# Kernel tuning notes

Hardware: AMD Instinct MI355X
Metric: run time of the kernel (lower is better)

The kernel has to match this reference:

```python
import jax, jax.numpy as jnp
import numpy as np

# AutoNCP(units=512, output_size=64) layer sizes (per ncps AutoNCP formula):
# inter_and_command = 512-64 = 448; command = max(int(0.4*448),1) = 179;
# inter = 448-179 = 269; motor = 64.
INPUT_DIM = 74  # LATENT(64)+ACTION(8)+CLICK(2), hard-coded in source
INTER, COMMAND, MOTOR = 269, 179, 64
BATCH = 65536
DENSITY = 0.5  # AutoNCP default density_level


def _make_layer(key, in_dim, hid):
    # CfCCell params (backbone_layers=0 => cat_shape = in_dim + hid).
    ks = jax.random.split(key, 9)
    s = 1.0 / np.sqrt(in_dim + hid)
    def W(k):
        return jax.random.uniform(k, (in_dim + hid, hid), minval=-s, maxval=s, dtype=jnp.float32)
    def b(k):
        return jax.random.uniform(k, (hid,), minval=-s, maxval=s, dtype=jnp.float32)
    # sparsity mask: sensory/inter part is sparse (~density), recurrent part is all ones
    # (WiredCfCCell concatenates a ones block for the hidden-state columns).
    top = (jax.random.uniform(ks[8], (in_dim, hid)) < DENSITY).astype(jnp.int32)
    mask = jnp.concatenate([top, jnp.ones((hid, hid), jnp.int32)], axis=0)  # [in+hid, hid]
    return dict(Wf1=W(ks[0]), bf1=b(ks[1]), Wf2=W(ks[2]), bf2=b(ks[3]),
                Wta=W(ks[4]), bta=b(ks[5]), Wtb=W(ks[6]), btb=b(ks[7]), mask=mask)


def setup_inputs() -> dict:
    key = jax.random.key(0)
    kx, k0, k1, k2 = jax.random.split(key, 4)
    inp = {"x": jax.random.normal(kx, (BATCH, INPUT_DIM), dtype=jnp.float32)}
    for i, (kk, in_dim, hid) in enumerate([(k0, INPUT_DIM, INTER), (k1, INTER, COMMAND), (k2, COMMAND, MOTOR)]):
        p = _make_layer(kk, in_dim, hid)
        for name, v in p.items():
            inp[f"{name}_{i}"] = v
    return inp


def _cfc_cell(x_in, h, mask, Wf1, bf1, Wf2, bf2, Wta, bta, Wtb, btb, ts=1.0):
    # x = cat([input, hx]); ff1/ff2 use sparsity-masked weights; time_a/time_b dense.
    xx = jnp.concatenate([x_in, h], axis=1)           # [B, in+hid]
    m = mask.astype(xx.dtype)
    ff1 = jnp.tanh(xx @ (Wf1 * m) + bf1)
    ff2 = jnp.tanh(xx @ (Wf2 * m) + bf2)
    t_a = xx @ Wta + bta
    t_b = xx @ Wtb + btb
    t_interp = jax.nn.sigmoid(-t_a * ts + t_b)        # closed-form time gate
    return ff1 * (1.0 - t_interp) + t_interp * ff2


def reference(x,
              Wf1_0, bf1_0, Wf2_0, bf2_0, Wta_0, bta_0, Wtb_0, btb_0, mask_0,
              Wf1_1, bf1_1, Wf2_1, bf2_1, Wta_1, bta_1, Wtb_1, btb_1, mask_1,
              Wf1_2, bf1_2, Wf2_2, bf2_2, Wta_2, bta_2, Wtb_2, btb_2, mask_2):
    B = x.shape[0]
    # seq_len = 1, zero initial hidden state, ts = 1.0 (CfC default elapsed time)
    h0 = jnp.zeros((B, INTER), x.dtype)
    h1 = jnp.zeros((B, COMMAND), x.dtype)
    h2 = jnp.zeros((B, MOTOR), x.dtype)
    o0 = _cfc_cell(x,  h0, mask_0, Wf1_0, bf1_0, Wf2_0, bf2_0, Wta_0, bta_0, Wtb_0, btb_0)
    o1 = _cfc_cell(o0, h1, mask_1, Wf1_1, bf1_1, Wf2_1, bf2_1, Wta_1, bta_1, Wtb_1, btb_1)
    o2 = _cfc_cell(o1, h2, mask_2, Wf1_2, bf1_2, Wf2_2, bf2_2, Wta_2, bta_2, Wtb_2, btb_2)
    return o2  # out[:, -1, :] -> motor neurons, [B, 64]
```

## Files before the change

### kernel.cpp

```cpp
#include <hip/hip_runtime.h>
#include <hip/hip_fp16.h>

typedef _Float16 f16x8 __attribute__((ext_vector_type(8)));
typedef _Float16 f16x4 __attribute__((ext_vector_type(4)));
typedef _Float16 f16x2 __attribute__((ext_vector_type(2)));
typedef float    f32x4 __attribute__((ext_vector_type(4)));

#define BM 64

#define IN0 74
#define H0  269
#define H1  179
#define H2  64
#define KS0 3
#define KS1 9
#define KS2 6
#define NP0 272
#define NP1 192
#define NP2 64
#define PX  104
#define PH0 296
#define PH1 200

#define MFMA16(a, b, c) __builtin_amdgcn_mfma_f32_16x16x32_f16(a, b, c, 0, 0, 0)

__device__ __forceinline__ float rform(float y) {
  return __builtin_amdgcn_rcpf(1.f + __expf(y));
}

template<int KS, int NP, int HID, int IPITCH, int OPITCH, bool LAST, int S, int G>
__device__ __forceinline__ void layer_run(
    const _Float16* in_lds, _Float16* out_lds, float* out_g,
    const _Float16* __restrict__ wt, int lane, int wid)
{
  constexpr int NT = NP / 16;
  const int l15 = lane & 15;
  const int lg  = lane >> 4;
  #pragma unroll 1
  for (int u = wid; u < NT * G; u += 8) {
    const int t     = u / G;
    const int mbase = (u % G) * (S * 16);
    const _Float16* a_base = in_lds + (mbase + l15) * IPITCH + lg * 8;
    const _Float16* wtt = wt + (size_t)(t * KS * 3) * 512 + lane * 8;

    f32x4 acc[3][S] = {};
    f16x8 b0 = *(const f16x8*)(wtt);
    f16x8 b1 = *(const f16x8*)(wtt + 512);
    f16x8 b2 = *(const f16x8*)(wtt + 1024);
    #pragma unroll 1
    for (int ks = 0; ks < KS - 1; ++ks) {
      const _Float16* wn = wtt + (size_t)(ks + 1) * 1536;
      f16x8 n0 = *(const f16x8*)(wn);
      f16x8 n1 = *(const f16x8*)(wn + 512);
      f16x8 n2 = *(const f16x8*)(wn + 1024);
      #pragma unroll
      for (int s = 0; s < S; ++s) {
        f16x8 a = *(const f16x8*)(a_base + s * 16 * IPITCH + ks * 32);
        acc[0][s] = MFMA16(b0, a, acc[0][s]);
        acc[1][s] = MFMA16(b1, a, acc[1][s]);
        acc[2][s] = MFMA16(b2, a, acc[2][s]);
      }
      b0 = n0; b1 = n1; b2 = n2;
    }
    #pragma unroll
    for (int s = 0; s < S; ++s) {
      f16x8 a = *(const f16x8*)(a_base + s * 16 * IPITCH + (KS - 1) * 32);
      acc[0][s] = MFMA16(b0, a, acc[0][s]);
      acc[1][s] = MFMA16(b1, a, acc[1][s]);
      acc[2][s] = MFMA16(b2, a, acc[2][s]);
    }

    const int nb = t * 16 + lg * 4;
    #pragma unroll
    for (int s = 0; s < S; ++s) {
      const int m = mbase + s * 16 + l15;
      float o[4];
      #pragma unroll
      for (int q = 0; q < 4; ++q) {
        float r1 = rform(acc[0][s][q]);
        float r2 = rform(acc[1][s][q]);
        float ti = rform(-acc[2][s][q]);
        o[q] = 1.f - 2.f * (r1 - ti * (r1 - r2));
      }
      if (LAST) {
        float4 v = make_float4(o[0], o[1], o[2], o[3]);
        *(float4*)(out_g + m * 64 + nb) = v;
      } else if (nb + 4 <= HID) {
        f16x4 h = {(_Float16)o[0], (_Float16)o[1], (_Float16)o[2], (_Float16)o[3]};
        *(f16x4*)(out_lds + m * OPITCH + nb) = h;
      } else {
        #pragma unroll
        for (int q = 0; q < 4; ++q)
          if (nb + q < HID) out_lds[m * OPITCH + nb + q] = (_Float16)o[q];
      }
    }
  }
}

__global__ __launch_bounds__(512, 4) void cfc_fused(
    const float* __restrict__ x,
    const _Float16* __restrict__ wt0, const _Float16* __restrict__ wt1,
    const _Float16* __restrict__ wt2,
    float* __restrict__ out)
{
  __shared__ __align__(16) _Float16 xs [BM * PX];
  __shared__ __align__(16) _Float16 h0s[BM * PH0];
  __shared__ __align__(16) _Float16 h1s[BM * PH1];
  const int tid  = threadIdx.x;
  const int lane = tid & 63;
  const int wid  = tid >> 6;
  const int m0 = blockIdx.x * BM;

  for (int i = tid; i < BM * 22; i += 512) { int r = i / 22, c = IN0 + i - r * 22; xs [r * PX  + c] = (_Float16)(c == IN0 ? 1.f : 0.f); }
  for (int i = tid; i < BM * 19; i += 512) { int r = i / 19, c = H0  + i - r * 19; h0s[r * PH0 + c] = (_Float16)(c == H0  ? 1.f : 0.f); }
  for (int i = tid; i < BM * 13; i += 512) { int r = i / 13, c = H1  + i - r * 13; h1s[r * PH1 + c] = (_Float16)(c == H1  ? 1.f : 0.f); }

  for (int i = tid; i < BM * 37; i += 512) {
    int r = i / 37, p = i - r * 37;
    float2 v = ((const float2*)x)[(size_t)(m0 + r) * 37 + p];
    f16x2 hv = {(_Float16)v.x, (_Float16)v.y};
    *(f16x2*)(xs + r * PX + 2 * p) = hv;
  }
  __syncthreads();

  layer_run<KS0, NP0, H0, PX,  PH0, false, 4, 1>(xs,  h0s, nullptr, wt0, lane, wid);
  __syncthreads();
  layer_run<KS1, NP1, H1, PH0, PH1, false, 4, 1>(h0s, h1s, nullptr, wt1, lane, wid);
  __syncthreads();
  layer_run<KS2, NP2, H2, PH1, 1,   true,  2, 2>(h1s, nullptr, out + (size_t)m0 * 64,
                                                 wt2, lane, wid);
}

__global__ void pack_w(const float* __restrict__ wf1, const float* __restrict__ wf2,
                       const float* __restrict__ wta, const float* __restrict__ wtb,
                       const float* __restrict__ bf1, const float* __restrict__ bf2,
                       const float* __restrict__ bta, const float* __restrict__ btb,
                       const int* __restrict__ mask, _Float16* __restrict__ wt,
                       int IN, int HID, int KS, int NT)
{
  int idx = blockIdx.x * 256 + threadIdx.x;
  int total = NT * KS * 3 * 64;
  if (idx >= total) return;
  int lane = idx & 63;
  int c = idx >> 6;
  int m = c % 3;
  int tk = c / 3;
  int ks = tk % KS;
  int t  = tk / KS;
  int n  = t * 16 + (lane & 15);
  int k0 = ks * 32 + (lane >> 4) * 8;
  f16x8 v = {};
  if (n < HID) {
    #pragma unroll
    for (int j = 0; j < 8; ++j) {
      int k = k0 + j;
      float f = 0.f;
      if (k < IN) {
        if (m == 0)      f = 2.f * wf1[k * HID + n] * (float)mask[k * HID + n];
        else if (m == 1) f = 2.f * wf2[k * HID + n] * (float)mask[k * HID + n];
        else             f = wtb[k * HID + n] - wta[k * HID + n];
      } else if (k == IN) {
        if (m == 0)      f = 2.f * bf1[n];
        else if (m == 1) f = 2.f * bf2[n];
        else             f = btb[n] - bta[n];
      }
      v[j] = (_Float16)f;
    }
  }
  *(f16x8*)(wt + (size_t)idx * 8) = v;
}

extern "C" void kernel_launch(void* const* d_in, const int* in_sizes, int n_in,
                              void* d_out, int out_size, void* d_ws, size_t ws_size,
                              hipStream_t stream)
{
  const float* x = (const float*)d_in[0];
  const float* Wf1_0 = (const float*)d_in[1];
  const float* bf1_0 = (const float*)d_in[2];
  const float* Wf2_0 = (const float*)d_in[3];
  const float* bf2_0 = (const float*)d_in[4];
  const float* Wta_0 = (const float*)d_in[5];
  const float* bta_0 = (const float*)d_in[6];
  const float* Wtb_0 = (const float*)d_in[7];
  const float* btb_0 = (const float*)d_in[8];
  const int*   msk_0 = (const int*)  d_in[9];
  const float* Wf1_1 = (const float*)d_in[10];
  const float* bf1_1 = (const float*)d_in[11];
  const float* Wf2_1 = (const float*)d_in[12];
  const float* bf2_1 = (const float*)d_in[13];
  const float* Wta_1 = (const float*)d_in[14];
  const float* bta_1 = (const float*)d_in[15];
  const float* Wtb_1 = (const float*)d_in[16];
  const float* btb_1 = (const float*)d_in[17];
  const int*   msk_1 = (const int*)  d_in[18];
  const float* Wf1_2 = (const float*)d_in[19];
  const float* bf1_2 = (const float*)d_in[20];
  const float* Wf2_2 = (const float*)d_in[21];
  const float* bf2_2 = (const float*)d_in[22];
  const float* Wta_2 = (const float*)d_in[23];
  const float* bta_2 = (const float*)d_in[24];
  const float* Wtb_2 = (const float*)d_in[25];
  const float* btb_2 = (const float*)d_in[26];
  const int*   msk_2 = (const int*)  d_in[27];

  char* ws = (char*)d_ws;
  _Float16* wt0 = (_Float16*)(ws + 0);
  _Float16* wt1 = (_Float16*)(ws + 156672);
  _Float16* wt2 = (_Float16*)(ws + 488448);

  pack_w<<<(17 * KS0 * 3 * 64 + 255) / 256, 256, 0, stream>>>(
      Wf1_0, Wf2_0, Wta_0, Wtb_0, bf1_0, bf2_0, bta_0, btb_0, msk_0, wt0, IN0, H0, KS0, 17);
  pack_w<<<(12 * KS1 * 3 * 64 + 255) / 256, 256, 0, stream>>>(
      Wf1_1, Wf2_1, Wta_1, Wtb_1, bf1_1, bf2_1, bta_1, btb_1, msk_1, wt1, H0, H1, KS1, 12);
  pack_w<<<( 4 * KS2 * 3 * 64 + 255) / 256, 256, 0, stream>>>(
      Wf1_2, Wf2_2, Wta_2, Wtb_2, bf1_2, bf2_2, bta_2, btb_2, msk_2, wt2, H1, H2, KS2, 4);

  cfc_fused<<<65536 / BM, 512, 0, stream>>>(x, wt0, wt1, wt2, (float*)d_out);
}
```

Before: 72.56 us.

## Double batch tile to 128 rows, 12 waves, two N-tiles per wave

Each block now handles 128 rows with 768 threads (12 waves), and every wave computes two adjacent 16-column N-tiles, so each A fragment loaded from LDS feeds six MFMAs instead of three. Layer 0 is padded to 288 columns so the tile count is even, and the weight workspace offsets are shifted to match. The double-buffered weight prefetch is dropped in favour of loading all six B fragments per k-step. The accumulator count doubles, which raises register pressure, and the larger LDS footprint plus 768-thread blocks lowers the number of resident blocks per CU.

```diff
diff --git a/kernel.cpp b/kernel.cpp
--- a/kernel.cpp
+++ b/kernel.cpp
@@ -6,7 +6,7 @@
 typedef _Float16 f16x2 __attribute__((ext_vector_type(2)));
 typedef float    f32x4 __attribute__((ext_vector_type(4)));
 
-#define BM 64
+#define BM 128
 
 #define IN0 74
 #define H0  269
@@ -15,12 +15,13 @@
 #define KS0 3
 #define KS1 9
 #define KS2 6
-#define NP0 272
+#define NP0 288
 #define NP1 192
 #define NP2 64
 #define PX  104
 #define PH0 296
 #define PH1 200
+#define WPB 12
 
 #define MFMA16(a, b, c) __builtin_amdgcn_mfma_f32_16x16x32_f16(a, b, c, 0, 0, 0)
 
@@ -33,71 +34,71 @@
     const _Float16* in_lds, _Float16* out_lds, float* out_g,
     const _Float16* __restrict__ wt, int lane, int wid)
 {
-  constexpr int NT = NP / 16;
+  constexpr int NPR = NP / 32;
   const int l15 = lane & 15;
   const int lg  = lane >> 4;
   #pragma unroll 1
-  for (int u = wid; u < NT * G; u += 8) {
-    const int t     = u / G;
+  for (int u = wid; u < NPR * G; u += WPB) {
+    const int p     = u / G;
     const int mbase = (u % G) * (S * 16);
     const _Float16* a_base = in_lds + (mbase + l15) * IPITCH + lg * 8;
-    const _Float16* wtt = wt + (size_t)(t * KS * 3) * 512 + lane * 8;
-
-    f32x4 acc[3][S] = {};
-    f16x8 b0 = *(const f16x8*)(wtt);
-    f16x8 b1 = *(const f16x8*)(wtt + 512);
-    f16x8 b2 = *(const f16x8*)(wtt + 1024);
+    const _Float16* w0 = wt + (size_t)(2 * p * KS * 3) * 512 + lane * 8;
+    const _Float16* w1 = w0 + (size_t)(KS * 3) * 512;
+
+    f32x4 acc[3][2][S] = {};
     #pragma unroll 1
-    for (int ks = 0; ks < KS - 1; ++ks) {
-      const _Float16* wn = wtt + (size_t)(ks + 1) * 1536;
-      f16x8 n0 = *(const f16x8*)(wn);
-      f16x8 n1 = *(const f16x8*)(wn + 512);
-      f16x8 n2 = *(const f16x8*)(wn + 1024);
+    for (int ks = 0; ks < KS; ++ks) {
+      const _Float16* k0p = w0 + (size_t)ks * 1536;
+      const _Float16* k1p = w1 + (size_t)ks * 1536;
+      f16x8 b00 = *(const f16x8*)(k0p);
+      f16x8 b01 = *(const f16x8*)(k0p + 512);
+      f16x8 b02 = *(const f16x8*)(k0p + 1024);
+      f16x8 b10 = *(const f16x8*)(k1p);
+      f16x8 b11 = *(const f16x8*)(k1p + 512);
+      f16x8 b12 = *(const f16x8*)(k1p + 1024);
       #pragma unroll
       for (int s = 0; s < S; ++s) {
         f16x8 a = *(const f16x8*)(a_base + s * 16 * IPITCH + ks * 32);
-        acc[0][s] = MFMA16(b0, a, acc[0][s]);
-        acc[1][s] = MFMA16(b1, a, acc[1][s]);
-        acc[2][s] = MFMA16(b2, a, acc[2][s]);
+        acc[0][0][s] = MFMA16(b00, a, acc[0][0][s]);
+        acc[1][0][s] = MFMA16(b01, a, acc[1][0][s]);
+        acc[2][0][s] = MFMA16(b02, a, acc[2][0][s]);
+        acc[0][1][s] = MFMA16(b10, a, acc[0][1][s]);
+        acc[1][1][s] = MFMA16(b11, a, acc[1][1][s]);
+        acc[2][1][s] = MFMA16(b12, a, acc[2][1][s]);
       }
-      b0 = n0; b1 = n1; b2 = n2;
     }
+
     #pragma unroll
-    for (int s = 0; s < S; ++s) {
-      f16x8 a = *(const f16x8*)(a_base + s * 16 * IPITCH + (KS - 1) * 32);
-      acc[0][s] = MFMA16(b0, a, acc[0][s]);
-      acc[1][s] = MFMA16(b1, a, acc[1][s]);
-      acc[2][s] = MFMA16(b2, a, acc[2][s]);
-    }
-
-    const int nb = t * 16 + lg * 4;
-    #pragma unroll
-    for (int s = 0; s < S; ++s) {
-      const int m = mbase + s * 16 + l15;
-      float o[4];
+    for (int nt = 0; nt < 2; ++nt) {
+      const int nb = (2 * p + nt) * 16 + lg * 4;
       #pragma unroll
-      for (int q = 0; q < 4; ++q) {
-        float r1 = rform(acc[0][s][q]);
-        float r2 = rform(acc[1][s][q]);
-        float ti = rform(-acc[2][s][q]);
-        o[q] = 1.f - 2.f * (r1 - ti * (r1 - r2));
-      }
-      if (LAST) {
-        float4 v = make_float4(o[0], o[1], o[2], o[3]);
-        *(float4*)(out_g + m * 64 + nb) = v;
-      } else if (nb + 4 <= HID) {
-        f16x4 h = {(_Float16)o[0], (_Float16)o[1], (_Float16)o[2], (_Float16)o[3]};
-        *(f16x4*)(out_lds + m * OPITCH + nb) = h;
-      } else {
+      for (int s = 0; s < S; ++s) {
+        const int m = mbase + s * 16 + l15;
+        float o[4];
         #pragma unroll
-        for (int q = 0; q < 4; ++q)
-          if (nb + q < HID) out_lds[m * OPITCH + nb + q] = (_Float16)o[q];
+        for (int q = 0; q < 4; ++q) {
+          float r1 = rform(acc[0][nt][s][q]);
+          float r2 = rform(acc[1][nt][s][q]);
+          float ti = rform(-acc[2][nt][s][q]);
+          o[q] = 1.f - 2.f * (r1 - ti * (r1 - r2));
+        }
+        if (LAST) {
+          float4 v = make_float4(o[0], o[1], o[2], o[3]);
+          *(float4*)(out_g + m * 64 + nb) = v;
+        } else if (nb + 4 <= HID) {
+          f16x4 h = {(_Float16)o[0], (_Float16)o[1], (_Float16)o[2], (_Float16)o[3]};
+          *(f16x4*)(out_lds + m * OPITCH + nb) = h;
+        } else {
+          #pragma unroll
+          for (int q = 0; q < 4; ++q)
+            if (nb + q < HID) out_lds[m * OPITCH + nb + q] = (_Float16)o[q];
+        }
       }
     }
   }
 }
 
-__global__ __launch_bounds__(512, 4) void cfc_fused(
+__global__ __launch_bounds__(768, 3) void cfc_fused(
     const float* __restrict__ x,
     const _Float16* __restrict__ wt0, const _Float16* __restrict__ wt1,
     const _Float16* __restrict__ wt2,
@@ -111,11 +112,11 @@
   const int wid  = tid >> 6;
   const int m0 = blockIdx.x * BM;
 
-  for (int i = tid; i < BM * 22; i += 512) { int r = i / 22, c = IN0 + i - r * 22; xs [r * PX  + c] = (_Float16)(c == IN0 ? 1.f : 0.f); }
-  for (int i = tid; i < BM * 19; i += 512) { int r = i / 19, c = H0  + i - r * 19; h0s[r * PH0 + c] = (_Float16)(c == H0  ? 1.f : 0.f); }
-  for (int i = tid; i < BM * 13; i += 512) { int r = i / 13, c = H1  + i - r * 13; h1s[r * PH1 + c] = (_Float16)(c == H1  ? 1.f : 0.f); }
-
-  for (int i = tid; i < BM * 37; i += 512) {
+  for (int i = tid; i < BM * 22; i += 768) { int r = i / 22, c = IN0 + i - r * 22; xs [r * PX  + c] = (_Float16)(c == IN0 ? 1.f : 0.f); }
+  for (int i = tid; i < BM * 19; i += 768) { int r = i / 19, c = H0  + i - r * 19; h0s[r * PH0 + c] = (_Float16)(c == H0  ? 1.f : 0.f); }
+  for (int i = tid; i < BM * 13; i += 768) { int r = i / 13, c = H1  + i - r * 13; h1s[r * PH1 + c] = (_Float16)(c == H1  ? 1.f : 0.f); }
+
+  for (int i = tid; i < BM * 37; i += 768) {
     int r = i / 37, p = i - r * 37;
     float2 v = ((const float2*)x)[(size_t)(m0 + r) * 37 + p];
     f16x2 hv = {(_Float16)v.x, (_Float16)v.y};
@@ -123,11 +124,11 @@
   }
   __syncthreads();
 
-  layer_run<KS0, NP0, H0, PX,  PH0, false, 4, 1>(xs,  h0s, nullptr, wt0, lane, wid);
+  layer_run<KS0, NP0, H0, PX,  PH0, false, 4, 2>(xs,  h0s, nullptr, wt0, lane, wid);
   __syncthreads();
-  layer_run<KS1, NP1, H1, PH0, PH1, false, 4, 1>(h0s, h1s, nullptr, wt1, lane, wid);
+  layer_run<KS1, NP1, H1, PH0, PH1, false, 4, 2>(h0s, h1s, nullptr, wt1, lane, wid);
   __syncthreads();
-  layer_run<KS2, NP2, H2, PH1, 1,   true,  2, 2>(h1s, nullptr, out + (size_t)m0 * 64,
+  layer_run<KS2, NP2, H2, PH1, 1,   true,  2, 4>(h1s, nullptr, out + (size_t)m0 * 64,
                                                  wt2, lane, wid);
 }
 
@@ -205,15 +206,15 @@
 
   char* ws = (char*)d_ws;
   _Float16* wt0 = (_Float16*)(ws + 0);
-  _Float16* wt1 = (_Float16*)(ws + 156672);
-  _Float16* wt2 = (_Float16*)(ws + 488448);
-
-  pack_w<<<(17 * KS0 * 3 * 64 + 255) / 256, 256, 0, stream>>>(
-      Wf1_0, Wf2_0, Wta_0, Wtb_0, bf1_0, bf2_0, bta_0, btb_0, msk_0, wt0, IN0, H0, KS0, 17);
+  _Float16* wt1 = (_Float16*)(ws + 165888);
+  _Float16* wt2 = (_Float16*)(ws + 497664);
+
+  pack_w<<<(18 * KS0 * 3 * 64 + 255) / 256, 256, 0, stream>>>(
+      Wf1_0, Wf2_0, Wta_0, Wtb_0, bf1_0, bf2_0, bta_0, btb_0, msk_0, wt0, IN0, H0, KS0, 18);
   pack_w<<<(12 * KS1 * 3 * 64 + 255) / 256, 256, 0, stream>>>(
       Wf1_1, Wf2_1, Wta_1, Wtb_1, bf1_1, bf2_1, bta_1, btb_1, msk_1, wt1, H0, H1, KS1, 12);
   pack_w<<<( 4 * KS2 * 3 * 64 + 255) / 256, 256, 0, stream>>>(
       Wf1_2, Wf2_2, Wta_2, Wtb_2, bf1_2, bf2_2, bta_2, btb_2, msk_2, wt2, H1, H2, KS2, 4);
 
-  cfc_fused<<<65536 / BM, 512, 0, stream>>>(x, wt0, wt1, wt2, (float*)d_out);
-}
+  cfc_fused<<<65536 / BM, 768, 0, stream>>>(x, wt0, wt1, wt2, (float*)d_out);
+}
```

Result: slower. 80.40 us (+10.8%).

## Halve row tile, raise occupancy, fold log2e into packed weights

Applied to the files above, without the earlier changes.

Cuts the per-block batch tile from 64 to 32 rows and halves the per-wave M subtiles. This shrinks LDS and registers so the launch bound can ask for 6 blocks per CU instead of 4. It also drops the software prefetch of the next K-slice of weights, which simplifies the loop but exposes global/L2 load latency. Separately, log2(e) is folded into the packed fp16 weights so the epilogue can use exp2 directly, at some risk of extra fp16 rounding and weight reloads per row tile.

```diff
diff --git a/kernel.cpp b/kernel.cpp
--- a/kernel.cpp
+++ b/kernel.cpp
@@ -6,7 +6,7 @@
 typedef _Float16 f16x2 __attribute__((ext_vector_type(2)));
 typedef float    f32x4 __attribute__((ext_vector_type(4)));
 
-#define BM 64
+#define BM 32
 
 #define IN0 74
 #define H0  269
@@ -24,8 +24,8 @@
 
 #define MFMA16(a, b, c) __builtin_amdgcn_mfma_f32_16x16x32_f16(a, b, c, 0, 0, 0)
 
-__device__ __forceinline__ float rform(float y) {
-  return __builtin_amdgcn_rcpf(1.f + __expf(y));
+__device__ __forceinline__ float rform2(float y) {
+  return __builtin_amdgcn_rcpf(1.f + exp2f(y));
 }
 
 template<int KS, int NP, int HID, int IPITCH, int OPITCH, bool LAST, int S, int G>
@@ -44,15 +44,12 @@
     const _Float16* wtt = wt + (size_t)(t * KS * 3) * 512 + lane * 8;
 
     f32x4 acc[3][S] = {};
-    f16x8 b0 = *(const f16x8*)(wtt);
-    f16x8 b1 = *(const f16x8*)(wtt + 512);
-    f16x8 b2 = *(const f16x8*)(wtt + 1024);
     #pragma unroll 1
-    for (int ks = 0; ks < KS - 1; ++ks) {
-      const _Float16* wn = wtt + (size_t)(ks + 1) * 1536;
-      f16x8 n0 = *(const f16x8*)(wn);
-      f16x8 n1 = *(const f16x8*)(wn + 512);
-      f16x8 n2 = *(const f16x8*)(wn + 1024);
+    for (int ks = 0; ks < KS; ++ks) {
+      const _Float16* wk = wtt + (size_t)ks * 1536;
+      f16x8 b0 = *(const f16x8*)(wk);
+      f16x8 b1 = *(const f16x8*)(wk + 512);
+      f16x8 b2 = *(const f16x8*)(wk + 1024);
       #pragma unroll
       for (int s = 0; s < S; ++s) {
         f16x8 a = *(const f16x8*)(a_base + s * 16 * IPITCH + ks * 32);
@@ -60,14 +57,6 @@
         acc[1][s] = MFMA16(b1, a, acc[1][s]);
         acc[2][s] = MFMA16(b2, a, acc[2][s]);
       }
-      b0 = n0; b1 = n1; b2 = n2;
-    }
-    #pragma unroll
-    for (int s = 0; s < S; ++s) {
-      f16x8 a = *(const f16x8*)(a_base + s * 16 * IPITCH + (KS - 1) * 32);
-      acc[0][s] = MFMA16(b0, a, acc[0][s]);
-      acc[1][s] = MFMA16(b1, a, acc[1][s]);
-      acc[2][s] = MFMA16(b2, a, acc[2][s]);
     }
 
     const int nb = t * 16 + lg * 4;
@@ -77,9 +66,9 @@
       float o[4];
       #pragma unroll
       for (int q = 0; q < 4; ++q) {
-        float r1 = rform(acc[0][s][q]);
-        float r2 = rform(acc[1][s][q]);
-        float ti = rform(-acc[2][s][q]);
+        float r1 = rform2(acc[0][s][q]);
+        float r2 = rform2(acc[1][s][q]);
+        float ti = rform2(-acc[2][s][q]);
         o[q] = 1.f - 2.f * (r1 - ti * (r1 - r2));
       }
       if (LAST) {
@@ -97,7 +86,7 @@
   }
 }
 
-__global__ __launch_bounds__(512, 4) void cfc_fused(
+__global__ __launch_bounds__(512, 6) void cfc_fused(
     const float* __restrict__ x,
     const _Float16* __restrict__ wt0, const _Float16* __restrict__ wt1,
     const _Float16* __restrict__ wt2,
@@ -123,11 +112,11 @@
   }
   __syncthreads();
 
-  layer_run<KS0, NP0, H0, PX,  PH0, false, 4, 1>(xs,  h0s, nullptr, wt0, lane, wid);
+  layer_run<KS0, NP0, H0, PX,  PH0, false, 2, 1>(xs,  h0s, nullptr, wt0, lane, wid);
   __syncthreads();
-  layer_run<KS1, NP1, H1, PH0, PH1, false, 4, 1>(h0s, h1s, nullptr, wt1, lane, wid);
+  layer_run<KS1, NP1, H1, PH0, PH1, false, 2, 1>(h0s, h1s, nullptr, wt1, lane, wid);
   __syncthreads();
-  layer_run<KS2, NP2, H2, PH1, 1,   true,  2, 2>(h1s, nullptr, out + (size_t)m0 * 64,
+  layer_run<KS2, NP2, H2, PH1, 1,   true,  1, 2>(h1s, nullptr, out + (size_t)m0 * 64,
                                                  wt2, lane, wid);
 }
 
@@ -138,6 +127,8 @@
                        const int* __restrict__ mask, _Float16* __restrict__ wt,
                        int IN, int HID, int KS, int NT)
 {
+  const float SC2 = 2.885390081777927f;
+  const float SC1 = 1.4426950408889634f;
   int idx = blockIdx.x * 256 + threadIdx.x;
   int total = NT * KS * 3 * 64;
   if (idx >= total) return;
@@ -156,13 +147,13 @@
       int k = k0 + j;
       float f = 0.f;
       if (k < IN) {
-        if (m == 0)      f = 2.f * wf1[k * HID + n] * (float)mask[k * HID + n];
-        else if (m == 1) f = 2.f * wf2[k * HID + n] * (float)mask[k * HID + n];
-        else             f = wtb[k * HID + n] - wta[k * HID + n];
+        if (m == 0)      f = SC2 * wf1[k * HID + n] * (float)mask[k * HID + n];
+        else if (m == 1) f = SC2 * wf2[k * HID + n] * (float)mask[k * HID + n];
+        else             f = SC1 * (wtb[k * HID + n] - wta[k * HID + n]);
       } else if (k == IN) {
-        if (m == 0)      f = 2.f * bf1[n];
-        else if (m == 1) f = 2.f * bf2[n];
-        else             f = btb[n] - bta[n];
+        if (m == 0)      f = SC2 * bf1[n];
+        else if (m == 1) f = SC2 * bf2[n];
+        else             f = SC1 * (btb[n] - bta[n]);
       }
       v[j] = (_Float16)f;
     }
```

Result: slower. 83.40 us (+14.9%).
